# Optimization experiments

Hardware: AMD Instinct MI355X
Metric: run time of the kernel (lower is better)

Reference implementation:

```python
import jax, jax.numpy as jnp
import numpy as np

DT = 0.001
BATCH, INPUT_SIZE, HIDDEN_SIZE, T = 32, 16384, 1024, 10


def setup_inputs() -> dict:
    key = jax.random.key(0)
    k1, k2, k3 = jax.random.split(key, 3)
    input_spikes = (jax.random.uniform(k1, (BATCH, INPUT_SIZE, T)) < 0.1).astype(jnp.float32)
    weight = jax.random.normal(k2, (INPUT_SIZE, HIDDEN_SIZE), dtype=jnp.float32) * 0.1
    synaptic_strength = jnp.ones((INPUT_SIZE, HIDDEN_SIZE), jnp.float32)
    threshold = jnp.ones((HIDDEN_SIZE,), jnp.float32)  # threshold_init = 1.0
    firing_rate_estimate = jnp.zeros((HIDDEN_SIZE,), jnp.float32)
    return {
        "input_spikes": input_spikes,
        "weight": weight,
        "synaptic_strength": synaptic_strength,
        "threshold": threshold,
        "firing_rate_estimate": firing_rate_estimate,
        "tau_mem": jnp.float32(0.02),
        "tau_syn": jnp.float32(0.005),
        "target_rate": jnp.float32(0.1),
        "homeostatic_lr": jnp.float32(0.001),
        "time_steps": T,
    }


def reference(input_spikes, weight, synaptic_strength, threshold,
              firing_rate_estimate, tau_mem, tau_syn, target_rate,
              homeostatic_lr, time_steps):
    # input_spikes: [B, I, T]; eval mode (no stochastic STDP branch)
    B = input_spikes.shape[0]
    H = threshold.shape[0]
    alpha_mem = jnp.exp(-DT / tau_mem)
    alpha_syn = jnp.exp(-DT / tau_syn)
    # precompute the per-step weighted input once: [T, B, H]
    w_eff = weight * synaptic_strength
    weighted = jnp.einsum('bit,ih->tbh', input_spikes[..., :time_steps], w_eff)

    def step(carry, w_in):
        v, i, fre, thr = carry
        i = alpha_syn * i + w_in
        v = alpha_mem * v + i
        spikes = (v >= thr[None, :]).astype(v.dtype)
        v = v - spikes * thr[None, :]  # reset_mode='subtract'
        spike_rate = spikes.mean(axis=0)
        fre = 0.99 * fre + 0.01 * spike_rate
        thr = thr + homeostatic_lr * (fre - target_rate)  # homeostatic adaptation
        diag = (v.mean(), spike_rate.mean(), thr.mean())
        return (v, i, fre, thr), (spikes, diag)

    init = (jnp.zeros((B, H), input_spikes.dtype),
            jnp.zeros((B, H), input_spikes.dtype),
            firing_rate_estimate, threshold)
    _, (spikes_tbh, (mem_means, rate_means, thr_means)) = jax.lax.scan(step, init, weighted)
    output_spikes = jnp.transpose(spikes_tbh, (1, 2, 0))  # [B, H, T]
    return output_spikes, mem_means, rate_means, thr_means
```

## Files before the change

### kernel.cpp

```cpp
#include <hip/hip_runtime.h>
#include <stdint.h>

#define B_ 32
#define I_ 16384
#define H_ 1024
#define T_ 10
#define M_ 320
#define NW 32

typedef __attribute__((ext_vector_type(8))) short short8;
typedef __attribute__((ext_vector_type(4))) float f32x4;
typedef __attribute__((ext_vector_type(4))) unsigned int u32x4;

__global__ __launch_bounds__(256) void pack_s(const float* __restrict__ spikes,
                                              uint16_t* __restrict__ Sbf) {
  __shared__ __align__(16) uint16_t tile[M_ * 40];
  const int i0 = blockIdx.x * 32;
#pragma unroll
  for (int p = 0; p < 10; p++) {
    int e = p * 256 + threadIdx.x;
    int b = e / 80;
    int r = e - b * 80;
    f32x4 val = *(const f32x4*)&spikes[(size_t)b * (I_ * T_) + (size_t)i0 * T_ + r * 4];
#pragma unroll
    for (int j = 0; j < 4; j++) {
      int pos = r * 4 + j;
      int il = pos / 10;
      int t = pos - il * 10;
      float f = (j == 0) ? val.x : (j == 1) ? val.y : (j == 2) ? val.z : val.w;
      union { float f; unsigned int u; } cv; cv.f = f;
      tile[(t * 32 + b) * 40 + il] = (uint16_t)(cv.u >> 16);
    }
  }
  __syncthreads();
#pragma unroll
  for (int p = 0; p < 5; p++) {
    int e = p * 256 + threadIdx.x;
    int m = e >> 2, il8 = e & 3;
    u32x4 w = *(const u32x4*)&tile[m * 40 + il8 * 8];
    *(u32x4*)&Sbf[(size_t)m * I_ + i0 + il8 * 8] = w;
  }
}

__global__ __launch_bounds__(640, 5) void gemm(const uint16_t* __restrict__ Sbf,
                                               const float* __restrict__ Wg,
                                               const float* __restrict__ Sg,
                                               float* __restrict__ partial,
                                               int kchunk) {
  __shared__ __align__(16) uint16_t WhiL[2][NW * 40];
  __shared__ __align__(16) uint16_t WloL[2][NW * 40];

  const int nt = blockIdx.x & 31;
  const int ks = blockIdx.x >> 5;
  const int nbase = nt * NW;
  const int tid = threadIdx.x;
  const int lane = tid & 63, wid = tid >> 6;
  const int quad = lane >> 4, l15 = lane & 15;

  const int stages = kchunk >> 5;
  const int kofs = ks * kchunk;

  const uint16_t* aptr0 = Sbf + (size_t)(wid * 32 + l15) * I_ + quad * 8;
  const uint16_t* aptr1 = aptr0 + (size_t)16 * I_;

  const int wn = tid & 31;
  const int wko = (tid >> 5) & 3;

  f32x4 acc[2][2];
#pragma unroll
  for (int a = 0; a < 2; a++)
#pragma unroll
    for (int b = 0; b < 2; b++) acc[a][b] = f32x4{0.f, 0.f, 0.f, 0.f};

  u32x4 afA[2], afB[2];
  float wpre[8], spre[8];

#define PACK_W(pn)                                                          \
  if (tid < 128) {                                                          \
    unsigned int hw[4], lw[4];                                              \
    _Pragma("unroll")                                                       \
    for (int j2 = 0; j2 < 4; j2++) {                                        \
      unsigned int hh[2], ll[2];                                            \
      _Pragma("unroll")                                                     \
      for (int e = 0; e < 2; e++) {                                         \
        float p = wpre[j2 * 2 + e] * spre[j2 * 2 + e];                      \
        union { float f; unsigned int u; } cv; cv.f = p;                    \
        unsigned int hb = (cv.u + 0x7FFFu + ((cv.u >> 16) & 1u)) >> 16;     \
        union { unsigned int u; float f; } hv; hv.u = hb << 16;             \
        float lo = p - hv.f;                                                \
        union { float f; unsigned int u; } cl; cl.f = lo;                   \
        unsigned int lb = (cl.u + 0x7FFFu + ((cl.u >> 16) & 1u)) >> 16;     \
        hh[e] = hb; ll[e] = lb;                                             \
      }                                                                     \
      hw[j2] = hh[0] | (hh[1] << 16);                                       \
      lw[j2] = ll[0] | (ll[1] << 16);                                       \
    }                                                                       \
    *(u32x4*)&WhiL[pn][wn * 40 + wko * 8] = u32x4{hw[0], hw[1], hw[2], hw[3]}; \
    *(u32x4*)&WloL[pn][wn * 40 + wko * 8] = u32x4{lw[0], lw[1], lw[2], lw[3]}; \
  }

#define LOAD_W(kb)                                                          \
  if (tid < 128) {                                                          \
    _Pragma("unroll")                                                       \
    for (int j = 0; j < 8; j++) {                                           \
      size_t g = (size_t)((kb) + wko * 8 + j) * H_ + nbase + wn;            \
      wpre[j] = Wg[g]; spre[j] = Sg[g];                                     \
    }                                                                       \
  }

#define COMPUTE(AF, pc)                                                     \
  {                                                                         \
    short8 a0 = __builtin_bit_cast(short8, AF[0]);                          \
    short8 a1 = __builtin_bit_cast(short8, AF[1]);                          \
    _Pragma("unroll")                                                       \
    for (int tn = 0; tn < 2; tn++) {                                        \
      int n = tn * 16 + l15;                                                \
      short8 bhi = *(const short8*)&WhiL[pc][n * 40 + quad * 8];            \
      short8 blo = *(const short8*)&WloL[pc][n * 40 + quad * 8];            \
      acc[0][tn] = __builtin_amdgcn_mfma_f32_16x16x32_bf16(a0, bhi, acc[0][tn], 0, 0, 0); \
      acc[0][tn] = __builtin_amdgcn_mfma_f32_16x16x32_bf16(a0, blo, acc[0][tn], 0, 0, 0); \
      acc[1][tn] = __builtin_amdgcn_mfma_f32_16x16x32_bf16(a1, bhi, acc[1][tn], 0, 0, 0); \
      acc[1][tn] = __builtin_amdgcn_mfma_f32_16x16x32_bf16(a1, blo, acc[1][tn], 0, 0, 0); \
    }                                                                       \
  }

  afA[0] = *(const u32x4*)(aptr0 + kofs);
  afA[1] = *(const u32x4*)(aptr1 + kofs);
  LOAD_W(kofs);
  PACK_W(0);
  {
    int s1 = (1 < stages) ? 1 : 0;
    int k1 = kofs + (s1 << 5);
    afB[0] = *(const u32x4*)(aptr0 + k1);
    afB[1] = *(const u32x4*)(aptr1 + k1);
    LOAD_W(k1);
  }
  __syncthreads();

  for (int s = 0; s < stages; s += 2) {
    COMPUTE(afA, 0);
    PACK_W(1);
    {
      int s2 = s + 2; if (s2 >= stages) s2 = stages - 1;
      int k2 = kofs + (s2 << 5);
      afA[0] = *(const u32x4*)(aptr0 + k2);
      afA[1] = *(const u32x4*)(aptr1 + k2);
      LOAD_W(k2);
    }
    __syncthreads();
    COMPUTE(afB, 1);
    PACK_W(0);
    {
      int s3 = s + 3; if (s3 >= stages) s3 = stages - 1;
      int k3 = kofs + (s3 << 5);
      afB[0] = *(const u32x4*)(aptr0 + k3);
      afB[1] = *(const u32x4*)(aptr1 + k3);
      LOAD_W(k3);
    }
    __syncthreads();
  }

#pragma unroll
  for (int tm = 0; tm < 2; tm++)
#pragma unroll
    for (int tn = 0; tn < 2; tn++) {
      int mrow = wid * 32 + tm * 16 + quad * 4;
      int ncol = nbase + tn * 16 + l15;
      float* dst = partial + ((size_t)ks * M_ + mrow) * H_ + ncol;
      dst[0 * H_] = acc[tm][tn].x;
      dst[1 * H_] = acc[tm][tn].y;
      dst[2 * H_] = acc[tm][tn].z;
      dst[3 * H_] = acc[tm][tn].w;
    }
#undef PACK_W
#undef LOAD_W
#undef COMPUTE
}

__global__ __launch_bounds__(256) void reduce_w(const float* __restrict__ partial,
                                                float* __restrict__ weighted,
                                                float* __restrict__ out, int KS) {
  if (blockIdx.x == 0 && threadIdx.x < 30) out[327680 + threadIdx.x] = 0.f;
  int j = (blockIdx.x * 256 + threadIdx.x) * 4;
  f32x4 s = f32x4{0.f, 0.f, 0.f, 0.f};
  for (int k = 0; k < KS; k++) {
    f32x4 p = *(const f32x4*)&partial[(size_t)k * (M_ * H_) + j];
    s += p;
  }
  *(f32x4*)&weighted[j] = s;
}

__global__ __launch_bounds__(64) void scan(const float* __restrict__ weighted,
                                           const float* __restrict__ threshold,
                                           const float* __restrict__ fre0,
                                           const float* __restrict__ p_tau_mem,
                                           const float* __restrict__ p_tau_syn,
                                           const float* __restrict__ p_target,
                                           const float* __restrict__ p_lr,
                                           float* __restrict__ out) {
  const int lane = threadIdx.x;
  const int hl = lane & 15, bg = lane >> 4;
  const int h = blockIdx.x * 16 + hl;
  const float alpha_mem = expf(-0.001f / p_tau_mem[0]);
  const float alpha_syn = expf(-0.001f / p_tau_syn[0]);
  const float target = p_target[0], lr = p_lr[0];
  float v[8], isyn[8];
#pragma unroll
  for (int j = 0; j < 8; j++) { v[j] = 0.f; isyn[j] = 0.f; }
  float fre = fre0[h];
  float thr = threshold[h];
  for (int t = 0; t < T_; t++) {
    float rsum = 0.f, vsum = 0.f;
#pragma unroll
    for (int j = 0; j < 8; j++) {
      int b = bg * 8 + j;
      float w_in = weighted[(size_t)(t * 32 + b) * H_ + h];
      isyn[j] = alpha_syn * isyn[j] + w_in;
      v[j] = alpha_mem * v[j] + isyn[j];
      float spike = (v[j] >= thr) ? 1.f : 0.f;
      v[j] -= spike * thr;
      out[(size_t)b * (H_ * T_) + (size_t)h * T_ + t] = spike;
      rsum += spike;
      vsum += v[j];
    }
    float r = rsum;
    r += __shfl_xor(r, 16);
    r += __shfl_xor(r, 32);
    float rate = r * (1.f / 32.f);
    fre = 0.99f * fre + 0.01f * rate;
    thr = thr + lr * (fre - target);
    float vv = vsum, rr = rate, tt = thr;
#pragma unroll
    for (int off = 32; off >= 1; off >>= 1) {
      vv += __shfl_xor(vv, off);
      rr += __shfl_xor(rr, off);
      tt += __shfl_xor(tt, off);
    }
    if (lane == 0) {
      atomicAdd(&out[327680 + t], vv * (1.f / 32768.f));
      atomicAdd(&out[327690 + t], rr * (1.f / 4096.f));
      atomicAdd(&out[327700 + t], tt * (1.f / 4096.f));
    }
  }
}

extern "C" void kernel_launch(void* const* d_in, const int* in_sizes, int n_in,
                              void* d_out, int out_size, void* d_ws, size_t ws_size,
                              hipStream_t stream) {
  const float* spikes    = (const float*)d_in[0];
  const float* weight    = (const float*)d_in[1];
  const float* strength  = (const float*)d_in[2];
  const float* threshold = (const float*)d_in[3];
  const float* fre0      = (const float*)d_in[4];
  const float* tau_mem   = (const float*)d_in[5];
  const float* tau_syn   = (const float*)d_in[6];
  const float* target    = (const float*)d_in[7];
  const float* lr        = (const float*)d_in[8];
  float* out = (float*)d_out;

  const size_t sbf_bytes = (size_t)M_ * I_ * 2;
  const size_t slice     = (size_t)M_ * H_ * 4;
  int KS = 16;
  while (KS > 1 && sbf_bytes + (size_t)(KS + 1) * slice > ws_size) KS >>= 1;

  uint16_t* Sbf   = (uint16_t*)d_ws;
  float* partial  = (float*)((char*)d_ws + sbf_bytes);
  float* weighted = (float*)((char*)d_ws + sbf_bytes + (size_t)KS * slice);

  pack_s<<<I_ / 32, 256, 0, stream>>>(spikes, Sbf);
  gemm<<<32 * KS, 640, 0, stream>>>(Sbf, weight, strength, partial, I_ / KS);
  reduce_w<<<(M_ * H_) / 1024, 256, 0, stream>>>(partial, weighted, out, KS);
  scan<<<H_ / 16, 64, 0, stream>>>(weighted, threshold, fre0, tau_mem, tau_syn,
                                   target, lr, out);
}
```

Measured before the change: 239.9 us.

## Restructure GEMM to register-direct W loads with larger M tiles, repack spikes

The GEMM drops its LDS staging of the bf16 hi/lo weight splits. Each wave now loads W and S straight from global memory into registers, converts them in registers, and computes an 80-row M tile (5x2 MFMA tiles) with 256-thread blocks and register double-buffering. This removes __syncthreads and the LDS traffic, at the cost of more redundant weight conversion across the four waves and higher register pressure. pack_s is rewritten without shared memory as direct strided gathers, and the scan uses 8 h-columns per block for more parallelism.

```diff
diff --git a/kernel.cpp b/kernel.cpp
--- a/kernel.cpp
+++ b/kernel.cpp
@@ -12,159 +12,121 @@
 typedef __attribute__((ext_vector_type(4))) float f32x4;
 typedef __attribute__((ext_vector_type(4))) unsigned int u32x4;
 
-__global__ __launch_bounds__(256) void pack_s(const float* __restrict__ spikes,
+__global__ __launch_bounds__(640) void pack_s(const float* __restrict__ spikes,
                                               uint16_t* __restrict__ Sbf) {
-  __shared__ __align__(16) uint16_t tile[M_ * 40];
-  const int i0 = blockIdx.x * 32;
-#pragma unroll
-  for (int p = 0; p < 10; p++) {
-    int e = p * 256 + threadIdx.x;
-    int b = e / 80;
-    int r = e - b * 80;
-    f32x4 val = *(const f32x4*)&spikes[(size_t)b * (I_ * T_) + (size_t)i0 * T_ + r * 4];
-#pragma unroll
-    for (int j = 0; j < 4; j++) {
-      int pos = r * 4 + j;
-      int il = pos / 10;
-      int t = pos - il * 10;
-      float f = (j == 0) ? val.x : (j == 1) ? val.y : (j == 2) ? val.z : val.w;
-      union { float f; unsigned int u; } cv; cv.f = f;
-      tile[(t * 32 + b) * 40 + il] = (uint16_t)(cv.u >> 16);
-    }
-  }
-  __syncthreads();
-#pragma unroll
-  for (int p = 0; p < 5; p++) {
-    int e = p * 256 + threadIdx.x;
-    int m = e >> 2, il8 = e & 3;
-    u32x4 w = *(const u32x4*)&tile[m * 40 + il8 * 8];
-    *(u32x4*)&Sbf[(size_t)m * I_ + i0 + il8 * 8] = w;
-  }
-}
-
-__global__ __launch_bounds__(640, 5) void gemm(const uint16_t* __restrict__ Sbf,
-                                               const float* __restrict__ Wg,
-                                               const float* __restrict__ Sg,
-                                               float* __restrict__ partial,
-                                               int kchunk) {
-  __shared__ __align__(16) uint16_t WhiL[2][NW * 40];
-  __shared__ __align__(16) uint16_t WloL[2][NW * 40];
-
-  const int nt = blockIdx.x & 31;
-  const int ks = blockIdx.x >> 5;
+  const int b = blockIdx.x & 31, imac = blockIdx.x >> 5;
+  const int t = threadIdx.x >> 6, lane = threadIdx.x & 63;
+  const int i0 = imac * 512 + lane * 8;
+  const float* sp = spikes + (size_t)b * (I_ * T_) + (size_t)i0 * T_ + t;
+  unsigned int w[4];
+#pragma unroll
+  for (int p = 0; p < 4; p++) {
+    union { float f; unsigned int u; } c0, c1;
+    c0.f = sp[(2 * p) * T_];
+    c1.f = sp[(2 * p + 1) * T_];
+    w[p] = (c0.u >> 16) | (c1.u & 0xFFFF0000u);
+  }
+  const int m = t * 32 + b;
+  *(u32x4*)&Sbf[(size_t)m * I_ + i0] = u32x4{w[0], w[1], w[2], w[3]};
+}
+
+__global__ __launch_bounds__(256) void gemm(const uint16_t* __restrict__ Sbf,
+                                            const float* __restrict__ Wg,
+                                            const float* __restrict__ Sg,
+                                            float* __restrict__ partial,
+                                            int kchunk, int kslog) {
+  const int ks = blockIdx.x & ((1 << kslog) - 1);
+  const int nt = blockIdx.x >> kslog;
   const int nbase = nt * NW;
   const int tid = threadIdx.x;
   const int lane = tid & 63, wid = tid >> 6;
   const int quad = lane >> 4, l15 = lane & 15;
-
+  const int kofs = ks * kchunk;
   const int stages = kchunk >> 5;
-  const int kofs = ks * kchunk;
-
-  const uint16_t* aptr0 = Sbf + (size_t)(wid * 32 + l15) * I_ + quad * 8;
-  const uint16_t* aptr1 = aptr0 + (size_t)16 * I_;
-
-  const int wn = tid & 31;
-  const int wko = (tid >> 5) & 3;
-
-  f32x4 acc[2][2];
-#pragma unroll
-  for (int a = 0; a < 2; a++)
+
+  const uint16_t* ap = Sbf + (size_t)(wid * 80 + l15) * I_ + quad * 8 + kofs;
+  const size_t boff = (size_t)(kofs + quad * 8) * H_ + nbase + l15;
+  const float* wp = Wg + boff;
+  const float* sp = Sg + boff;
+
+  f32x4 acc[5][2];
+#pragma unroll
+  for (int a = 0; a < 5; a++)
 #pragma unroll
     for (int b = 0; b < 2; b++) acc[a][b] = f32x4{0.f, 0.f, 0.f, 0.f};
 
-  u32x4 afA[2], afB[2];
-  float wpre[8], spre[8];
-
-#define PACK_W(pn)                                                          \
-  if (tid < 128) {                                                          \
-    unsigned int hw[4], lw[4];                                              \
+  u32x4 af0[5], af1[5];
+  float wv0[2][8], sv0[2][8], wv1[2][8], sv1[2][8];
+
+#define LOADS(af, wv, sv, sk)                                               \
+  {                                                                         \
+    const size_t ko = (size_t)(sk) * 32;                                    \
     _Pragma("unroll")                                                       \
-    for (int j2 = 0; j2 < 4; j2++) {                                        \
-      unsigned int hh[2], ll[2];                                            \
+    for (int tm = 0; tm < 5; tm++)                                          \
+      af[tm] = *(const u32x4*)(ap + (size_t)tm * 16 * I_ + ko);             \
+    _Pragma("unroll")                                                       \
+    for (int tn = 0; tn < 2; tn++)                                          \
       _Pragma("unroll")                                                     \
-      for (int e = 0; e < 2; e++) {                                         \
-        float p = wpre[j2 * 2 + e] * spre[j2 * 2 + e];                      \
-        union { float f; unsigned int u; } cv; cv.f = p;                    \
-        unsigned int hb = (cv.u + 0x7FFFu + ((cv.u >> 16) & 1u)) >> 16;     \
-        union { unsigned int u; float f; } hv; hv.u = hb << 16;             \
-        float lo = p - hv.f;                                                \
-        union { float f; unsigned int u; } cl; cl.f = lo;                   \
-        unsigned int lb = (cl.u + 0x7FFFu + ((cl.u >> 16) & 1u)) >> 16;     \
-        hh[e] = hb; ll[e] = lb;                                             \
+      for (int j = 0; j < 8; j++) {                                         \
+        size_t o = (ko + j) * H_ + tn * 16;                                 \
+        wv[tn][j] = wp[o];                                                  \
+        sv[tn][j] = sp[o];                                                  \
       }                                                                     \
-      hw[j2] = hh[0] | (hh[1] << 16);                                       \
-      lw[j2] = ll[0] | (ll[1] << 16);                                       \
-    }                                                                       \
-    *(u32x4*)&WhiL[pn][wn * 40 + wko * 8] = u32x4{hw[0], hw[1], hw[2], hw[3]}; \
-    *(u32x4*)&WloL[pn][wn * 40 + wko * 8] = u32x4{lw[0], lw[1], lw[2], lw[3]}; \
-  }
-
-#define LOAD_W(kb)                                                          \
-  if (tid < 128) {                                                          \
-    _Pragma("unroll")                                                       \
-    for (int j = 0; j < 8; j++) {                                           \
-      size_t g = (size_t)((kb) + wko * 8 + j) * H_ + nbase + wn;            \
-      wpre[j] = Wg[g]; spre[j] = Sg[g];                                     \
-    }                                                                       \
-  }
-
-#define COMPUTE(AF, pc)                                                     \
+  }
+
+#define COMPUTE(af, wv, sv)                                                 \
   {                                                                         \
-    short8 a0 = __builtin_bit_cast(short8, AF[0]);                          \
-    short8 a1 = __builtin_bit_cast(short8, AF[1]);                          \
     _Pragma("unroll")                                                       \
     for (int tn = 0; tn < 2; tn++) {                                        \
-      int n = tn * 16 + l15;                                                \
-      short8 bhi = *(const short8*)&WhiL[pc][n * 40 + quad * 8];            \
-      short8 blo = *(const short8*)&WloL[pc][n * 40 + quad * 8];            \
-      acc[0][tn] = __builtin_amdgcn_mfma_f32_16x16x32_bf16(a0, bhi, acc[0][tn], 0, 0, 0); \
-      acc[0][tn] = __builtin_amdgcn_mfma_f32_16x16x32_bf16(a0, blo, acc[0][tn], 0, 0, 0); \
-      acc[1][tn] = __builtin_amdgcn_mfma_f32_16x16x32_bf16(a1, bhi, acc[1][tn], 0, 0, 0); \
-      acc[1][tn] = __builtin_amdgcn_mfma_f32_16x16x32_bf16(a1, blo, acc[1][tn], 0, 0, 0); \
+      unsigned int hw[4], lw[4];                                            \
+      _Pragma("unroll")                                                     \
+      for (int p = 0; p < 4; p++) {                                         \
+        unsigned int hu[2], lu[2];                                          \
+        _Pragma("unroll")                                                   \
+        for (int e = 0; e < 2; e++) {                                       \
+          float pr = wv[tn][2 * p + e] * sv[tn][2 * p + e];                 \
+          union { float f; unsigned int u; } cv; cv.f = pr;                 \
+          unsigned int r = (cv.u + 0x7FFFu + ((cv.u >> 16) & 1u)) &        \
+                           0xFFFF0000u;                    \
+          union { unsigned int u; float f; } hv; hv.u = r;                  \
+          union { float f; unsigned int u; } cl; cl.f = pr - hv.f; \
+          unsigned int rl = (cl.u + 0x7FFFu + ((cl.u >> 16) & 1u)) &       \
+                            0xFFFF0000u;                   \
+          hu[e] = r; lu[e] = rl;                                            \
+        }                                                                   \
+        hw[p] = (hu[0] >> 16) | (hu[1] & 0xFFFF0000u);                      \
+        lw[p] = (lu[0] >> 16) | (lu[1] & 0xFFFF0000u);                      \
+      }                                                                     \
+      short8 bhi = __builtin_bit_cast(short8, u32x4{hw[0], hw[1], hw[2], hw[3]}); \
+      short8 blo = __builtin_bit_cast(short8, u32x4{lw[0], lw[1], lw[2], lw[3]}); \
+      _Pragma("unroll")                                                     \
+      for (int tm = 0; tm < 5; tm++) {                                      \
+        short8 av = __builtin_bit_cast(short8, af[tm]);                     \
+        acc[tm][tn] = __builtin_amdgcn_mfma_f32_16x16x32_bf16(av, bhi, acc[tm][tn], 0, 0, 0); \
+        acc[tm][tn] = __builtin_amdgcn_mfma_f32_16x16x32_bf16(av, blo, acc[tm][tn], 0, 0, 0); \
+      }                                                                     \
     }                                                                       \
   }
 
-  afA[0] = *(const u32x4*)(aptr0 + kofs);
-  afA[1] = *(const u32x4*)(aptr1 + kofs);
-  LOAD_W(kofs);
-  PACK_W(0);
-  {
-    int s1 = (1 < stages) ? 1 : 0;
-    int k1 = kofs + (s1 << 5);
-    afB[0] = *(const u32x4*)(aptr0 + k1);
-    afB[1] = *(const u32x4*)(aptr1 + k1);
-    LOAD_W(k1);
-  }
-  __syncthreads();
-
-  for (int s = 0; s < stages; s += 2) {
-    COMPUTE(afA, 0);
-    PACK_W(1);
-    {
-      int s2 = s + 2; if (s2 >= stages) s2 = stages - 1;
-      int k2 = kofs + (s2 << 5);
-      afA[0] = *(const u32x4*)(aptr0 + k2);
-      afA[1] = *(const u32x4*)(aptr1 + k2);
-      LOAD_W(k2);
-    }
-    __syncthreads();
-    COMPUTE(afB, 1);
-    PACK_W(0);
-    {
-      int s3 = s + 3; if (s3 >= stages) s3 = stages - 1;
-      int k3 = kofs + (s3 << 5);
-      afB[0] = *(const u32x4*)(aptr0 + k3);
-      afB[1] = *(const u32x4*)(aptr1 + k3);
-      LOAD_W(k3);
-    }
-    __syncthreads();
-  }
-
-#pragma unroll
-  for (int tm = 0; tm < 2; tm++)
+  LOADS(af0, wv0, sv0, 0);
+  LOADS(af1, wv1, sv1, 1);
+  int s = 0;
+  for (; s + 2 < stages; s += 2) {
+    COMPUTE(af0, wv0, sv0);
+    LOADS(af0, wv0, sv0, s + 2);
+    COMPUTE(af1, wv1, sv1);
+    LOADS(af1, wv1, sv1, s + 3);
+  }
+  COMPUTE(af0, wv0, sv0);
+  COMPUTE(af1, wv1, sv1);
+#undef LOADS
+#undef COMPUTE
+
+#pragma unroll
+  for (int tm = 0; tm < 5; tm++)
 #pragma unroll
     for (int tn = 0; tn < 2; tn++) {
-      int mrow = wid * 32 + tm * 16 + quad * 4;
+      int mrow = wid * 80 + tm * 16 + quad * 4;
       int ncol = nbase + tn * 16 + l15;
       float* dst = partial + ((size_t)ks * M_ + mrow) * H_ + ncol;
       dst[0 * H_] = acc[tm][tn].x;
@@ -172,9 +134,6 @@
       dst[2 * H_] = acc[tm][tn].z;
       dst[3 * H_] = acc[tm][tn].w;
     }
-#undef PACK_W
-#undef LOAD_W
-#undef COMPUTE
 }
 
 __global__ __launch_bounds__(256) void reduce_w(const float* __restrict__ partial,
@@ -199,21 +158,21 @@
                                            const float* __restrict__ p_lr,
                                            float* __restrict__ out) {
   const int lane = threadIdx.x;
-  const int hl = lane & 15, bg = lane >> 4;
-  const int h = blockIdx.x * 16 + hl;
+  const int hl = lane & 7, bg = lane >> 3;
+  const int h = blockIdx.x * 8 + hl;
   const float alpha_mem = expf(-0.001f / p_tau_mem[0]);
   const float alpha_syn = expf(-0.001f / p_tau_syn[0]);
   const float target = p_target[0], lr = p_lr[0];
-  float v[8], isyn[8];
-#pragma unroll
-  for (int j = 0; j < 8; j++) { v[j] = 0.f; isyn[j] = 0.f; }
+  float v[4], isyn[4];
+#pragma unroll
+  for (int j = 0; j < 4; j++) { v[j] = 0.f; isyn[j] = 0.f; }
   float fre = fre0[h];
   float thr = threshold[h];
   for (int t = 0; t < T_; t++) {
     float rsum = 0.f, vsum = 0.f;
 #pragma unroll
-    for (int j = 0; j < 8; j++) {
-      int b = bg * 8 + j;
+    for (int j = 0; j < 4; j++) {
+      int b = bg * 4 + j;
       float w_in = weighted[(size_t)(t * 32 + b) * H_ + h];
       isyn[j] = alpha_syn * isyn[j] + w_in;
       v[j] = alpha_mem * v[j] + isyn[j];
@@ -224,6 +183,7 @@
       vsum += v[j];
     }
     float r = rsum;
+    r += __shfl_xor(r, 8);
     r += __shfl_xor(r, 16);
     r += __shfl_xor(r, 32);
     float rate = r * (1.f / 32.f);
@@ -238,8 +198,8 @@
     }
     if (lane == 0) {
       atomicAdd(&out[327680 + t], vv * (1.f / 32768.f));
-      atomicAdd(&out[327690 + t], rr * (1.f / 4096.f));
-      atomicAdd(&out[327700 + t], tt * (1.f / 4096.f));
+      atomicAdd(&out[327690 + t], rr * (1.f / 8192.f));
+      atomicAdd(&out[327700 + t], tt * (1.f / 8192.f));
     }
   }
 }
@@ -260,16 +220,18 @@
 
   const size_t sbf_bytes = (size_t)M_ * I_ * 2;
   const size_t slice     = (size_t)M_ * H_ * 4;
-  int KS = 16;
-  while (KS > 1 && sbf_bytes + (size_t)(KS + 1) * slice > ws_size) KS >>= 1;
+  int KS = 16, kslog = 4;
+  while (KS > 1 && sbf_bytes + (size_t)(KS + 1) * slice > ws_size) {
+    KS >>= 1; kslog--;
+  }
 
   uint16_t* Sbf   = (uint16_t*)d_ws;
   float* partial  = (float*)((char*)d_ws + sbf_bytes);
   float* weighted = (float*)((char*)d_ws + sbf_bytes + (size_t)KS * slice);
 
-  pack_s<<<I_ / 32, 256, 0, stream>>>(spikes, Sbf);
-  gemm<<<32 * KS, 640, 0, stream>>>(Sbf, weight, strength, partial, I_ / KS);
+  pack_s<<<32 * (I_ / 512), 640, 0, stream>>>(spikes, Sbf);
+  gemm<<<32 * KS, 256, 0, stream>>>(Sbf, weight, strength, partial, I_ / KS, kslog);
   reduce_w<<<(M_ * H_) / 1024, 256, 0, stream>>>(partial, weighted, out, KS);
-  scan<<<H_ / 16, 64, 0, stream>>>(weighted, threshold, fre0, tau_mem, tau_syn,
-                                   target, lr, out);
-}
+  scan<<<H_ / 8, 64, 0, stream>>>(weighted, threshold, fre0, tau_mem, tau_syn,
+                                  target, lr, out);
+}
```

After: 293.8 us. 1.22x slower.
